# Kernel tuning notes

Measured on AMD Instinct MI355X. Metric: run time of the kernel, lower is better.

Reference implementation:

```python
import jax, jax.numpy as jnp
import numpy as np

WINDOW_SIZE = (8, 8, 8)
DIM = 256
NUM_HEADS = 8
NUM_WINDOWS = 16
BATCH = 128  # num_windows * B
N = int(np.prod(WINDOW_SIZE))  # 512


def _make_rpb_buffers(ws):
    space = len(ws)
    coords = [np.arange(-(w - 1), w, dtype=np.float32) for w in ws]
    rpb = np.stack(np.meshgrid(*coords, indexing='ij'))  # (space, 2w-1, ...)
    for i in range(space):
        rpb[i] = rpb[i] / (ws[i] - 1)
    rpb = np.moveaxis(rpb, 0, -1)[None]  # (1, ..., space)
    rpb = 8.0 * rpb
    rpb = np.sign(rpb) * np.log2(np.abs(rpb) + 1.0) / np.log2(8.0)
    grid = np.stack(np.meshgrid(*[np.arange(w) for w in ws], indexing='ij'))
    g = grid.reshape(space, -1).astype(np.int64)
    dists = g[:, :, None] - g[:, None, :]  # (space, N, N)
    for i in range(space):
        center = max(int(np.prod([2 * w - 1 for w in ws[i + 1:]])), 1)
        dists[i] = (dists[i] + ws[i] - 1) * center
    rpb_idx = dists.sum(0)  # (N, N)
    return rpb.astype(np.float32), rpb_idx.astype(np.int32)


def setup_inputs() -> dict:
    key = jax.random.key(0)
    ks = jax.random.split(key, 8)
    rpb_np, rpb_idx_np = _make_rpb_buffers(WINDOW_SIZE)
    s = 0.02
    return {
        'x': jax.random.normal(ks[0], (BATCH, N, DIM), dtype=jnp.float32),
        'mask': jnp.zeros((NUM_WINDOWS, N, N), dtype=jnp.float32),
        'qkv_w': jax.random.normal(ks[1], (3 * DIM, DIM), dtype=jnp.float32) * s,
        'proj_w': jax.random.normal(ks[2], (DIM, DIM), dtype=jnp.float32) * s,
        'proj_b': jnp.zeros((DIM,), dtype=jnp.float32),
        'cpb_w1': jax.random.normal(ks[3], (512, 3), dtype=jnp.float32) * s,
        'cpb_b1': jnp.zeros((512,), dtype=jnp.float32),
        'cpb_w2': jax.random.normal(ks[4], (NUM_HEADS, 512), dtype=jnp.float32) * s,
        'rpb': jnp.asarray(rpb_np),
        'rpb_idx': jnp.asarray(rpb_idx_np),
    }


def reference(x, mask, qkv_w, proj_w, proj_b, cpb_w1, cpb_b1, cpb_w2, rpb, rpb_idx):
    b, n, c = x.shape
    h = cpb_w2.shape[0]
    hd = c // h
    # qkv projection (no bias), split into q,k,v of shape (b, h, n, hd)
    qkv = jnp.einsum('bnc,oc->bno', x, qkv_w).reshape(b, n, 3, h, hd)
    qkv = jnp.transpose(qkv, (2, 0, 3, 1, 4))
    q, k, v = qkv[0], qkv[1], qkv[2]
    # continuous relative-position bias: MLP over log-spaced coords, gather, sigmoid
    hidden = jax.nn.relu(jnp.einsum('...d,od->...o', rpb, cpb_w1) + cpb_b1)
    table = jnp.einsum('...o,ho->...h', hidden, cpb_w2).reshape(-1, h)  # (prod(2w-1), h)
    rpb_bias = table[rpb_idx.reshape(-1)].reshape(n, n, h)
    rpb_bias = 16.0 * jax.nn.sigmoid(rpb_bias)
    rpb_bias = jnp.transpose(rpb_bias, (2, 0, 1))[None]  # (1, h, n, n)
    # mask (nw, n, n) -> (b, 1, n, n) via repeat along batch
    nw = mask.shape[0]
    m = jnp.tile(mask[:, None, :, :], (b // nw, 1, 1, 1))
    bias = m + rpb_bias  # (b, h, n, n)
    # scaled dot-product attention
    scale = 1.0 / jnp.sqrt(jnp.float32(hd))
    scores = jnp.einsum('bhqd,bhkd->bhqk', q, k) * scale + bias
    attn = jax.nn.softmax(scores, axis=-1)
    out = jnp.einsum('bhqk,bhkd->bhqd', attn, v)
    out = jnp.transpose(out, (0, 2, 1, 3)).reshape(b, n, c)
    out = jnp.einsum('bnc,oc->bno', out, proj_w) + proj_b
    return out
```

## Files before the change

### kernel.cpp

```cpp
#include <hip/hip_runtime.h>
#include <hip/hip_bf16.h>


using u16 = unsigned short;
using u32 = unsigned int;
typedef short bf16x4 __attribute__((ext_vector_type(4)));
typedef short bf16x8 __attribute__((ext_vector_type(8)));
typedef float f32x4 __attribute__((ext_vector_type(4)));

#define QSL 0.25503471f
#define LOG2E 1.44269504f
#define CMB_SHIFT 11.65f

static __device__ __forceinline__ u32 cvt_pk_bf16(float lo, float hi) {
  u32 r;
  asm("v_cvt_pk_bf16_f32 %0, %1, %2" : "=v"(r) : "v"(lo), "v"(hi));
  return r;
}

__global__ __launch_bounds__(512) void cpb_kernel(
    const float* __restrict__ rpb, const float* __restrict__ w1,
    const float* __restrict__ b1, const float* __restrict__ w2,
    float* __restrict__ table16) {
  __shared__ float hid[512];
  const int p = blockIdx.x;
  const int t = threadIdx.x;
  const float r0 = rpb[p * 3 + 0], r1 = rpb[p * 3 + 1], r2 = rpb[p * 3 + 2];
  float hv = fmaf(r0, w1[t * 3 + 0],
             fmaf(r1, w1[t * 3 + 1],
             fmaf(r2, w1[t * 3 + 2], b1[t])));
  hid[t] = fmaxf(hv, 0.0f);
  __syncthreads();
  const int h = t >> 6, lane = t & 63;
  float s = 0.0f;
#pragma unroll
  for (int u = 0; u < 8; ++u)
    s = fmaf(hid[lane + u * 64], w2[h * 512 + lane + u * 64], s);
#pragma unroll
  for (int off = 32; off > 0; off >>= 1) s += __shfl_down(s, off);
  if (lane == 0) table16[p * 8 + h] = 23.08312065f / (1.0f + __expf(-s));
}

__global__ __launch_bounds__(256) void cmb_kernel(
    const int* __restrict__ rpb_idx, const float* __restrict__ table16,
    const float* __restrict__ mask, u16* __restrict__ cmb) {
  const int ij0 = (blockIdx.x * 256 + threadIdx.x) * 4;
  const int w = blockIdx.y;
  const float4 m4 = *reinterpret_cast<const float4*>(mask + (size_t)w * 262144 + ij0);
  const int4 i4 = *reinterpret_cast<const int4*>(rpb_idx + ij0);
  float ta[8], tb[8], tc[8], td[8];
  *reinterpret_cast<float4*>(&ta[0]) = *reinterpret_cast<const float4*>(table16 + i4.x * 8);
  *reinterpret_cast<float4*>(&ta[4]) = *reinterpret_cast<const float4*>(table16 + i4.x * 8 + 4);
  *reinterpret_cast<float4*>(&tb[0]) = *reinterpret_cast<const float4*>(table16 + i4.y * 8);
  *reinterpret_cast<float4*>(&tb[4]) = *reinterpret_cast<const float4*>(table16 + i4.y * 8 + 4);
  *reinterpret_cast<float4*>(&tc[0]) = *reinterpret_cast<const float4*>(table16 + i4.z * 8);
  *reinterpret_cast<float4*>(&tc[4]) = *reinterpret_cast<const float4*>(table16 + i4.z * 8 + 4);
  *reinterpret_cast<float4*>(&td[0]) = *reinterpret_cast<const float4*>(table16 + i4.w * 8);
  *reinterpret_cast<float4*>(&td[4]) = *reinterpret_cast<const float4*>(table16 + i4.w * 8 + 4);
  const float b0 = m4.x * LOG2E - CMB_SHIFT;
  const float b1 = m4.y * LOG2E - CMB_SHIFT;
  const float b2 = m4.z * LOG2E - CMB_SHIFT;
  const float b3 = m4.w * LOG2E - CMB_SHIFT;
  u16* outp = cmb + (size_t)w * 8 * 262144 + ij0;
#pragma unroll
  for (int h = 0; h < 8; ++h) {
    uint2 o;
    o.x = cvt_pk_bf16(ta[h] + b0, tb[h] + b1);
    o.y = cvt_pk_bf16(tc[h] + b2, td[h] + b3);
    *reinterpret_cast<uint2*>(outp + (size_t)h * 262144) = o;
  }
}

__global__ __launch_bounds__(256) void qkv_mfma(
    const float* __restrict__ x, const float* __restrict__ w,
    u16* __restrict__ qbuf, u16* __restrict__ kbuf, u16* __restrict__ vbuf) {
  __shared__ u16 As[128 * 64];
  __shared__ u16 Bs[128 * 64];
  const int tid = threadIdx.x;
  const int flat = blockIdx.x;
  const int wrk = (flat & 7) * 384 + (flat >> 3);
  const int bm = wrk / 6;
  const int bn = wrk - bm * 6;
  const int m0 = bm * 128, n0 = bn * 128;
  const float scl = (bn < 2) ? QSL : 1.0f;
  const int lane = tid & 63, wid = tid >> 6;
  const int wm = wid >> 1, wn = wid & 1;
  const int lq = lane & 15, g = lane >> 4;
  const f32x4 fz = {0.f, 0.f, 0.f, 0.f};
  f32x4 acc[4][4];
#pragma unroll
  for (int i = 0; i < 4; ++i)
#pragma unroll
    for (int j = 0; j < 4; ++j) acc[i][j] = fz;

  const int r0 = tid >> 3;
  const int ch = tid & 7;
  const int sx = (ch ^ (r0 & 7)) << 3;

  float4 ga[4][2], gb[4][2];
  auto gload = [&](int k0) {
#pragma unroll
    for (int rr = 0; rr < 4; ++rr) {
      const int r = r0 + rr * 32;
      const float* ax = x + (size_t)(m0 + r) * 256 + k0 + ch * 8;
      ga[rr][0] = *reinterpret_cast<const float4*>(ax);
      ga[rr][1] = *reinterpret_cast<const float4*>(ax + 4);
      const float* bx = w + (size_t)(n0 + r) * 256 + k0 + ch * 8;
      gb[rr][0] = *reinterpret_cast<const float4*>(bx);
      gb[rr][1] = *reinterpret_cast<const float4*>(bx + 4);
    }
  };

  gload(0);
  for (int k0 = 0; k0 < 256; k0 += 64) {
    __syncthreads();
#pragma unroll
    for (int rr = 0; rr < 4; ++rr) {
      const int r = r0 + rr * 32;
      uint4 pk;
      pk.x = cvt_pk_bf16(ga[rr][0].x, ga[rr][0].y);
      pk.y = cvt_pk_bf16(ga[rr][0].z, ga[rr][0].w);
      pk.z = cvt_pk_bf16(ga[rr][1].x, ga[rr][1].y);
      pk.w = cvt_pk_bf16(ga[rr][1].z, ga[rr][1].w);
      *reinterpret_cast<uint4*>(&As[r * 64 + sx]) = pk;
      pk.x = cvt_pk_bf16(gb[rr][0].x * scl, gb[rr][0].y * scl);
      pk.y = cvt_pk_bf16(gb[rr][0].z * scl, gb[rr][0].w * scl);
      pk.z = cvt_pk_bf16(gb[rr][1].x * scl, gb[rr][1].y * scl);
      pk.w = cvt_pk_bf16(gb[rr][1].z * scl, gb[rr][1].w * scl);
      *reinterpret_cast<uint4*>(&Bs[r * 64 + sx]) = pk;
    }
    __syncthreads();
    if (k0 + 64 < 256) gload(k0 + 64);
#pragma unroll
    for (int ks = 0; ks < 2; ++ks) {
      bf16x8 xf[4], wf[4];
#pragma unroll
      for (int mt = 0; mt < 4; ++mt) {
        const int row = wm * 64 + mt * 16 + lq;
        xf[mt] = *reinterpret_cast<const bf16x8*>(
            &As[row * 64 + (((ks * 4 + g) ^ (row & 7)) << 3)]);
      }
#pragma unroll
      for (int nt = 0; nt < 4; ++nt) {
        const int row = wn * 64 + nt * 16 + lq;
        wf[nt] = *reinterpret_cast<const bf16x8*>(
            &Bs[row * 64 + (((ks * 4 + g) ^ (row & 7)) << 3)]);
      }
#pragma unroll
      for (int mt = 0; mt < 4; ++mt)
#pragma unroll
        for (int nt = 0; nt < 4; ++nt)
          acc[mt][nt] = __builtin_amdgcn_mfma_f32_16x16x32_bf16(
              wf[nt], xf[mt], acc[mt][nt], 0, 0, 0);
    }
  }
  const int sec = bn >> 1;
  u16* dst = sec == 0 ? qbuf : (sec == 1 ? kbuf : vbuf);
#pragma unroll
  for (int mt = 0; mt < 4; ++mt) {
    const int m = m0 + wm * 64 + mt * 16 + lq;
    const int b = m >> 9, ii = m & 511;
#pragma unroll
    for (int nt = 0; nt < 4; ++nt) {
      const int n = n0 + wn * 64 + nt * 16 + 4 * g;
      const int h = (n & 255) >> 5;
      const int d = n & 31;
      const size_t off = ((size_t)(b * 8 + h) * 512 + ii) * 32 + d;
      uint2 o2;
      o2.x = cvt_pk_bf16(acc[mt][nt][0], acc[mt][nt][1]);
      o2.y = cvt_pk_bf16(acc[mt][nt][2], acc[mt][nt][3]);
      *reinterpret_cast<uint2*>(dst + off) = o2;
    }
  }
}

__global__ __launch_bounds__(256, 2) void attn_mfma(
    u16* qbuf,
    const u16* __restrict__ kbuf, const u16* __restrict__ vbuf,
    const u16* __restrict__ cmb) {
  __shared__ u16 Klds[512 * 32];
  __shared__ u16 Vtlds[32 * 512];
  const int t = threadIdx.x;
  const int qc = blockIdx.x, h = blockIdx.y;
  const int bz = blockIdx.z;
  const int b = ((bz & 15) << 3) | (bz >> 4);
  const size_t bh = (size_t)b * 8 + h;
  const u16* kb = kbuf + bh * 16384;
  const u16* vb = vbuf + bh * 16384;

#pragma unroll
  for (int c = 0; c < 8; ++c) {
    const int cid = t + c * 256;
    const int key = cid >> 2, ch = cid & 3;
    const uint4 kd = *reinterpret_cast<const uint4*>(kb + cid * 8);
    const int idx = key * 32 + ((ch * 8) ^ (((key >> 1) & 3) << 3));
    *reinterpret_cast<uint4*>(&Klds[idx]) = kd;
  }
#pragma unroll
  for (int r = 0; r < 2; ++r) {
    const int n = t + r * 256;
    const uint4 v0 = *reinterpret_cast<const uint4*>(vb + n * 32);
    const uint4 v1 = *reinterpret_cast<const uint4*>(vb + n * 32 + 8);
    const uint4 v2 = *reinterpret_cast<const uint4*>(vb + n * 32 + 16);
    const uint4 v3 = *reinterpret_cast<const uint4*>(vb + n * 32 + 24);
    const u32 wv16[16] = {v0.x, v0.y, v0.z, v0.w, v1.x, v1.y, v1.z, v1.w,
                          v2.x, v2.y, v2.z, v2.w, v3.x, v3.y, v3.z, v3.w};
#pragma unroll
    for (int u = 0; u < 16; ++u) {
      const int d0 = 2 * u, d1 = 2 * u + 1;
      Vtlds[d0 * 512 + (n ^ ((d0 & 7) << 3))] = (u16)(wv16[u] & 0xffffu);
      Vtlds[d1 * 512 + (n ^ ((d1 & 7) << 3))] = (u16)(wv16[u] >> 16);
    }
  }
  __syncthreads();

  const int lane = t & 63;
  const int lq = lane & 15, g = lane >> 4;
  const int wv = t >> 6;
  const int q0 = qc * 256 + wv * 64;

  bf16x8 Qf[4];
  u16* qrowbase = qbuf + bh * 16384;
#pragma unroll
  for (int qt = 0; qt < 4; ++qt)
    Qf[qt] = *reinterpret_cast<const bf16x8*>(qrowbase + (q0 + qt * 16 + lq) * 32 + g * 8);

  const u16* cmbp[4];
  const size_t whbase = (size_t)((b & 15) * 8 + h) * 262144;
#pragma unroll
  for (int qt = 0; qt < 4; ++qt)
    cmbp[qt] = cmb + whbase + (size_t)(q0 + qt * 16 + lq) * 512 + 4 * g;

  const f32x4 fzero = {0.f, 0.f, 0.f, 0.f};
  f32x4 o[2][4];
  f32x4 lsum4[4];
#pragma unroll
  for (int qt = 0; qt < 4; ++qt) {
    lsum4[qt] = fzero;
    o[0][qt] = fzero;
    o[1][qt] = fzero;
  }

  for (int j0 = 0; j0 < 512; j0 += 64) {
    bf16x8 Ak[4];
#pragma unroll
    for (int kt = 0; kt < 4; ++kt) {
      const int key = j0 + kt * 16 + lq;
      const int idx = key * 32 + ((g * 8) ^ (((key >> 1) & 3) << 3));
      Ak[kt] = *reinterpret_cast<const bf16x8*>(&Klds[idx]);
    }
    f32x4 s[4][4];
#pragma unroll
    for (int kt = 0; kt < 4; ++kt)
#pragma unroll
      for (int qt = 0; qt < 4; ++qt) {
        const uint2 cc = *reinterpret_cast<const uint2*>(cmbp[qt] + j0 + kt * 16);
        f32x4 ci;
        ci[0] = __uint_as_float((cc.x & 0xffffu) << 16);
        ci[1] = __uint_as_float(cc.x & 0xffff0000u);
        ci[2] = __uint_as_float((cc.y & 0xffffu) << 16);
        ci[3] = __uint_as_float(cc.y & 0xffff0000u);
        s[kt][qt] = __builtin_amdgcn_mfma_f32_16x16x32_bf16(Ak[kt], Qf[qt], ci, 0, 0, 0);
      }
#pragma unroll
    for (int kt = 0; kt < 4; ++kt) {
      bf16x4 Av[2];
#pragma unroll
      for (int dt = 0; dt < 2; ++dt) {
        const int d = dt * 16 + lq;
        const int n0 = j0 + kt * 16 + 4 * g;
        const int idx = d * 512 + (n0 ^ ((d & 7) << 3));
        Av[dt] = *reinterpret_cast<const bf16x4*>(&Vtlds[idx]);
      }
#pragma unroll
      for (int qt = 0; qt < 4; ++qt) {
        f32x4 p = s[kt][qt];
        p[0] = __builtin_amdgcn_exp2f(p[0]);
        p[1] = __builtin_amdgcn_exp2f(p[1]);
        p[2] = __builtin_amdgcn_exp2f(p[2]);
        p[3] = __builtin_amdgcn_exp2f(p[3]);
        lsum4[qt] += p;
        union { u32 u[2]; bf16x4 v; } bp;
        bp.u[0] = cvt_pk_bf16(p[0], p[1]);
        bp.u[1] = cvt_pk_bf16(p[2], p[3]);
        o[0][qt] = __builtin_amdgcn_mfma_f32_16x16x16bf16_1k(Av[0], bp.v, o[0][qt], 0, 0, 0);
        o[1][qt] = __builtin_amdgcn_mfma_f32_16x16x16bf16_1k(Av[1], bp.v, o[1][qt], 0, 0, 0);
      }
    }
  }
#pragma unroll
  for (int qt = 0; qt < 4; ++qt) {
    float l = (lsum4[qt][0] + lsum4[qt][1]) + (lsum4[qt][2] + lsum4[qt][3]);
    l += __shfl_xor(l, 16);
    l += __shfl_xor(l, 32);
    const float inv = 1.0f / l;
    u16* orow = qrowbase + (q0 + qt * 16 + lq) * 32;
#pragma unroll
    for (int dt = 0; dt < 2; ++dt) {
      uint2 w2;
      w2.x = cvt_pk_bf16(o[dt][qt][0] * inv, o[dt][qt][1] * inv);
      w2.y = cvt_pk_bf16(o[dt][qt][2] * inv, o[dt][qt][3] * inv);
      *reinterpret_cast<uint2*>(orow + dt * 16 + 4 * g) = w2;
    }
  }
}

__global__ __launch_bounds__(256) void proj_mfma(
    const u16* __restrict__ abuf, const float* __restrict__ w,
    const float* __restrict__ pb, float* __restrict__ out) {
  __shared__ u16 As[128 * 64];
  __shared__ u16 Bs[128 * 64];
  const int tid = threadIdx.x;
  const int bn = blockIdx.x;
  const int bm = blockIdx.y;
  const int m0 = bm * 128, n0 = bn * 128;
  const int lane = tid & 63, wid = tid >> 6;
  const int wm = wid >> 1, wn = wid & 1;
  const int lq = lane & 15, g = lane >> 4;
  const f32x4 fz = {0.f, 0.f, 0.f, 0.f};
  f32x4 acc[4][4];
#pragma unroll
  for (int i = 0; i < 4; ++i)
#pragma unroll
    for (int j = 0; j < 4; ++j) acc[i][j] = fz;

  const int r0 = tid >> 3;
  const int ch = tid & 7;
  const int sx = (ch ^ (r0 & 7)) << 3;
  const int ab = m0 >> 9;
  const u16* abase = abuf + (size_t)ab * 8 * 16384;
  const int dA0 = (ch & 3) * 8;

  uint4 gaq[4];
  float4 gb[4][2];
  auto gload = [&](int k0) {
    const int hA0 = (k0 >> 5) + (ch >> 2);
#pragma unroll
    for (int rr = 0; rr < 4; ++rr) {
      const int r = r0 + rr * 32;
      gaq[rr] = *reinterpret_cast<const uint4*>(
          abase + ((size_t)hA0 * 512 + ((m0 & 511) + r)) * 32 + dA0);
      const float* bx = w + (size_t)(n0 + r) * 256 + k0 + ch * 8;
      gb[rr][0] = *reinterpret_cast<const float4*>(bx);
      gb[rr][1] = *reinterpret_cast<const float4*>(bx + 4);
    }
  };

  gload(0);
  for (int k0 = 0; k0 < 256; k0 += 64) {
    __syncthreads();
#pragma unroll
    for (int rr = 0; rr < 4; ++rr) {
      const int r = r0 + rr * 32;
      *reinterpret_cast<uint4*>(&As[r * 64 + sx]) = gaq[rr];
      uint4 pk;
      pk.x = cvt_pk_bf16(gb[rr][0].x, gb[rr][0].y);
      pk.y = cvt_pk_bf16(gb[rr][0].z, gb[rr][0].w);
      pk.z = cvt_pk_bf16(gb[rr][1].x, gb[rr][1].y);
      pk.w = cvt_pk_bf16(gb[rr][1].z, gb[rr][1].w);
      *reinterpret_cast<uint4*>(&Bs[r * 64 + sx]) = pk;
    }
    __syncthreads();
    if (k0 + 64 < 256) gload(k0 + 64);
#pragma unroll
    for (int ks = 0; ks < 2; ++ks) {
      bf16x8 xf[4], wf[4];
#pragma unroll
      for (int mt = 0; mt < 4; ++mt) {
        const int row = wm * 64 + mt * 16 + lq;
        xf[mt] = *reinterpret_cast<const bf16x8*>(
            &As[row * 64 + (((ks * 4 + g) ^ (row & 7)) << 3)]);
      }
#pragma unroll
      for (int nt = 0; nt < 4; ++nt) {
        const int row = wn * 64 + nt * 16 + lq;
        wf[nt] = *reinterpret_cast<const bf16x8*>(
            &Bs[row * 64 + (((ks * 4 + g) ^ (row & 7)) << 3)]);
      }
#pragma unroll
      for (int mt = 0; mt < 4; ++mt)
#pragma unroll
        for (int nt = 0; nt < 4; ++nt)
          acc[mt][nt] = __builtin_amdgcn_mfma_f32_16x16x32_bf16(
              wf[nt], xf[mt], acc[mt][nt], 0, 0, 0);
    }
  }
#pragma unroll
  for (int mt = 0; mt < 4; ++mt) {
    const int m = m0 + wm * 64 + mt * 16 + lq;
#pragma unroll
    for (int nt = 0; nt < 4; ++nt) {
      const int n = n0 + wn * 64 + nt * 16 + 4 * g;
      const float4 pb4 = *reinterpret_cast<const float4*>(pb + n);
      *reinterpret_cast<float4*>(out + (size_t)m * 256 + n) =
          make_float4(acc[mt][nt][0] + pb4.x, acc[mt][nt][1] + pb4.y,
                      acc[mt][nt][2] + pb4.z, acc[mt][nt][3] + pb4.w);
    }
  }
}

extern "C" void kernel_launch(void* const* d_in, const int* in_sizes, int n_in,
                              void* d_out, int out_size, void* d_ws, size_t ws_size,
                              hipStream_t stream) {
  const float* x = (const float*)d_in[0];
  const float* mask = (const float*)d_in[1];
  const float* qkv_w = (const float*)d_in[2];
  const float* proj_w = (const float*)d_in[3];
  const float* proj_b = (const float*)d_in[4];
  const float* cpb_w1 = (const float*)d_in[5];
  const float* cpb_b1 = (const float*)d_in[6];
  const float* cpb_w2 = (const float*)d_in[7];
  const float* rpb = (const float*)d_in[8];
  const int* rpb_idx = (const int*)d_in[9];
  float* out = (float*)d_out;

  char* ws = (char*)d_ws;
  u16* qbuf = (u16*)(ws);
  u16* kbuf = (u16*)(ws + 33554432);
  u16* vbuf = (u16*)(ws + 67108864);
  u16* cmb = (u16*)(ws + 100663296);
  float* table16 = (float*)(ws + 167772160);

  cpb_kernel<<<3375, 512, 0, stream>>>(rpb, cpb_w1, cpb_b1, cpb_w2, table16);
  cmb_kernel<<<dim3(256, 16), 256, 0, stream>>>(rpb_idx, table16, mask, cmb);
  qkv_mfma<<<3072, 256, 0, stream>>>(x, qkv_w, qbuf, kbuf, vbuf);
  attn_mfma<<<dim3(2, 8, 128), 256, 0, stream>>>(qbuf, kbuf, vbuf, cmb);
  proj_mfma<<<dim3(2, 512), 256, 0, stream>>>(qbuf, proj_w, proj_b, out);
}
```

Baseline: 287.4 us.

## Widen proj GEMM tile to full 256 output columns per block

The output projection now has each block compute all 256 output columns for its 128 rows, using two B tiles and two accumulator sets. The A tile (attention output) is loaded once per block instead of twice across two column blocks. The register prefetch of the next k-slice is removed, so global loads are no longer overlapped with MFMA work, and launch bounds of 256 threads with 2 blocks per unit are added. The change doubles accumulator registers and LDS per block and halves the grid to 512 blocks, which may cut occupancy.

New measurement: 275.6 us. 1.04x faster.

```diff
diff --git a/kernel.cpp b/kernel.cpp
--- a/kernel.cpp
+++ b/kernel.cpp
@@ -305,24 +305,24 @@
   }
 }
 
-__global__ __launch_bounds__(256) void proj_mfma(
+__global__ __launch_bounds__(256, 2) void proj_mfma(
     const u16* __restrict__ abuf, const float* __restrict__ w,
     const float* __restrict__ pb, float* __restrict__ out) {
   __shared__ u16 As[128 * 64];
-  __shared__ u16 Bs[128 * 64];
+  __shared__ u16 Bs0[128 * 64];
+  __shared__ u16 Bs1[128 * 64];
   const int tid = threadIdx.x;
-  const int bn = blockIdx.x;
-  const int bm = blockIdx.y;
-  const int m0 = bm * 128, n0 = bn * 128;
+  const int bm = blockIdx.x;
+  const int m0 = bm * 128;
   const int lane = tid & 63, wid = tid >> 6;
   const int wm = wid >> 1, wn = wid & 1;
   const int lq = lane & 15, g = lane >> 4;
   const f32x4 fz = {0.f, 0.f, 0.f, 0.f};
-  f32x4 acc[4][4];
+  f32x4 acc0[4][4], acc1[4][4];
 #pragma unroll
   for (int i = 0; i < 4; ++i)
 #pragma unroll
-    for (int j = 0; j < 4; ++j) acc[i][j] = fz;
+    for (int j = 0; j < 4; ++j) { acc0[i][j] = fz; acc1[i][j] = fz; }
 
   const int r0 = tid >> 3;
   const int ch = tid & 7;
@@ -331,40 +331,33 @@
   const u16* abase = abuf + (size_t)ab * 8 * 16384;
   const int dA0 = (ch & 3) * 8;
 
-  uint4 gaq[4];
-  float4 gb[4][2];
-  auto gload = [&](int k0) {
+  for (int k0 = 0; k0 < 256; k0 += 64) {
     const int hA0 = (k0 >> 5) + (ch >> 2);
+    __syncthreads();
 #pragma unroll
     for (int rr = 0; rr < 4; ++rr) {
       const int r = r0 + rr * 32;
-      gaq[rr] = *reinterpret_cast<const uint4*>(
+      const uint4 ga = *reinterpret_cast<const uint4*>(
           abase + ((size_t)hA0 * 512 + ((m0 & 511) + r)) * 32 + dA0);
-      const float* bx = w + (size_t)(n0 + r) * 256 + k0 + ch * 8;
-      gb[rr][0] = *reinterpret_cast<const float4*>(bx);
-      gb[rr][1] = *reinterpret_cast<const float4*>(bx + 4);
-    }
-  };
-
-  gload(0);
-  for (int k0 = 0; k0 < 256; k0 += 64) {
+      const float* bx0 = w + (size_t)r * 256 + k0 + ch * 8;
+      const float* bx1 = w + (size_t)(128 + r) * 256 + k0 + ch * 8;
+      const float4 b00 = *reinterpret_cast<const float4*>(bx0);
+      const float4 b01 = *reinterpret_cast<const float4*>(bx0 + 4);
+      const float4 b10 = *reinterpret_cast<const float4*>(bx1);
+      const float4 b11 = *reinterpret_cast<const float4*>(bx1 + 4);
+      *reinterpret_cast<uint4*>(&As[r * 64 + sx]) = ga;
+      uint4 pk;
+      pk.x = cvt_pk_bf16(b00.x, b00.y); pk.y = cvt_pk_bf16(b00.z, b00.w);
+      pk.z = cvt_pk_bf16(b01.x, b01.y); pk.w = cvt_pk_bf16(b01.z, b01.w);
+      *reinterpret_cast<uint4*>(&Bs0[r * 64 + sx]) = pk;
+      pk.x = cvt_pk_bf16(b10.x, b10.y); pk.y = cvt_pk_bf16(b10.z, b10.w);
+      pk.z = cvt_pk_bf16(b11.x, b11.y); pk.w = cvt_pk_bf16(b11.z, b11.w);
+      *reinterpret_cast<uint4*>(&Bs1[r * 64 + sx]) = pk;
+    }
     __syncthreads();
 #pragma unroll
-    for (int rr = 0; rr < 4; ++rr) {
-      const int r = r0 + rr * 32;
-      *reinterpret_cast<uint4*>(&As[r * 64 + sx]) = gaq[rr];
-      uint4 pk;
-      pk.x = cvt_pk_bf16(gb[rr][0].x, gb[rr][0].y);
-      pk.y = cvt_pk_bf16(gb[rr][0].z, gb[rr][0].w);
-      pk.z = cvt_pk_bf16(gb[rr][1].x, gb[rr][1].y);
-      pk.w = cvt_pk_bf16(gb[rr][1].z, gb[rr][1].w);
-      *reinterpret_cast<uint4*>(&Bs[r * 64 + sx]) = pk;
-    }
-    __syncthreads();
-    if (k0 + 64 < 256) gload(k0 + 64);
-#pragma unroll
     for (int ks = 0; ks < 2; ++ks) {
-      bf16x8 xf[4], wf[4];
+      bf16x8 xf[4];
 #pragma unroll
       for (int mt = 0; mt < 4; ++mt) {
         const int row = wm * 64 + mt * 16 + lq;
@@ -374,15 +367,17 @@
 #pragma unroll
       for (int nt = 0; nt < 4; ++nt) {
         const int row = wn * 64 + nt * 16 + lq;
-        wf[nt] = *reinterpret_cast<const bf16x8*>(
-            &Bs[row * 64 + (((ks * 4 + g) ^ (row & 7)) << 3)]);
-      }
-#pragma unroll
-      for (int mt = 0; mt < 4; ++mt)
-#pragma unroll
-        for (int nt = 0; nt < 4; ++nt)
-          acc[mt][nt] = __builtin_amdgcn_mfma_f32_16x16x32_bf16(
-              wf[nt], xf[mt], acc[mt][nt], 0, 0, 0);
+        const int off = row * 64 + (((ks * 4 + g) ^ (row & 7)) << 3);
+        const bf16x8 wf0 = *reinterpret_cast<const bf16x8*>(&Bs0[off]);
+        const bf16x8 wf1 = *reinterpret_cast<const bf16x8*>(&Bs1[off]);
+#pragma unroll
+        for (int mt = 0; mt < 4; ++mt) {
+          acc0[mt][nt] = __builtin_amdgcn_mfma_f32_16x16x32_bf16(
+              wf0, xf[mt], acc0[mt][nt], 0, 0, 0);
+          acc1[mt][nt] = __builtin_amdgcn_mfma_f32_16x16x32_bf16(
+              wf1, xf[mt], acc1[mt][nt], 0, 0, 0);
+        }
+      }
     }
   }
 #pragma unroll
@@ -390,11 +385,15 @@
     const int m = m0 + wm * 64 + mt * 16 + lq;
 #pragma unroll
     for (int nt = 0; nt < 4; ++nt) {
-      const int n = n0 + wn * 64 + nt * 16 + 4 * g;
-      const float4 pb4 = *reinterpret_cast<const float4*>(pb + n);
+      const int n = wn * 64 + nt * 16 + 4 * g;
+      const float4 pb0 = *reinterpret_cast<const float4*>(pb + n);
       *reinterpret_cast<float4*>(out + (size_t)m * 256 + n) =
-          make_float4(acc[mt][nt][0] + pb4.x, acc[mt][nt][1] + pb4.y,
-                      acc[mt][nt][2] + pb4.z, acc[mt][nt][3] + pb4.w);
+          make_float4(acc0[mt][nt][0] + pb0.x, acc0[mt][nt][1] + pb0.y,
+                      acc0[mt][nt][2] + pb0.z, acc0[mt][nt][3] + pb0.w);
+      const float4 pb1 = *reinterpret_cast<const float4*>(pb + 128 + n);
+      *reinterpret_cast<float4*>(out + (size_t)m * 256 + 128 + n) =
+          make_float4(acc1[mt][nt][0] + pb1.x, acc1[mt][nt][1] + pb1.y,
+                      acc1[mt][nt][2] + pb1.z, acc1[mt][nt][3] + pb1.w);
     }
   }
 }
@@ -425,5 +424,5 @@
   cmb_kernel<<<dim3(256, 16), 256, 0, stream>>>(rpb_idx, table16, mask, cmb);
   qkv_mfma<<<3072, 256, 0, stream>>>(x, qkv_w, qbuf, kbuf, vbuf);
   attn_mfma<<<dim3(2, 8, 128), 256, 0, stream>>>(qbuf, kbuf, vbuf, cmb);
-  proj_mfma<<<dim3(2, 512), 256, 0, stream>>>(qbuf, proj_w, proj_b, out);
-}
+  proj_mfma<<<512, 256, 0, stream>>>(qbuf, proj_w, proj_b, out);
+}
```
